# Kernel tuning notes

Measured on AMD Instinct MI355X. Metric: run time of the kernel, lower is better.

Reference implementation:

```python
import jax, jax.numpy as jnp
import numpy as np

B = 64
N_TEXT, N_VIS, N_AC = 256, 32, 32
N = N_TEXT + N_VIS + N_AC  # 320 total graph nodes
HID, HEADS, LAYERS = 512, 8, 2
HEAD_DIM = HID // HEADS
SW_K, SW_P, SF_M, ALPHA, CROSS_P = 6, 0.15, 3, 0.5, 0.3


def build_hybrid_adj():
    """Watts-Strogatz + Barabasi-Albert hybrid adjacency with cross-modal edges (numpy, setup only)."""
    rng = np.random.default_rng(0)
    # small-world ring lattice
    sw = np.zeros((N, N), np.float32)
    idx = np.arange(N)
    for j in range(1, SW_K // 2 + 1):
        sw[idx, (idx + j) % N] = 1.0
        sw[idx, (idx - j) % N] = 1.0
    # rewiring
    for i in range(N):
        for j in range(i + 1, N):
            if sw[i, j] == 1 and rng.random() < SW_P:
                sw[i, j] = sw[j, i] = 0.0
                cand = np.where(sw[i] == 0)[0]
                cand = cand[cand != i]
                if len(cand) > 0:
                    nj = rng.choice(cand)
                    sw[i, nj] = sw[nj, i] = 1.0
    # scale-free (Barabasi-Albert)
    sf = np.zeros((N, N), np.float32)
    for i in range(SF_M + 1):
        for j in range(i + 1, SF_M + 1):
            sf[i, j] = sf[j, i] = 1.0
    deg = sf.sum(1)
    for v in range(SF_M + 1, N):
        prob = deg[:v] / deg[:v].sum()
        targets = rng.choice(v, size=min(SF_M, v), replace=False, p=prob)
        sf[v, targets] = 1.0
        sf[targets, v] = 1.0
        deg = sf.sum(1)
    adj = ((ALPHA * sw + (1.0 - ALPHA) * sf) > 0.3).astype(np.float32)
    # cross-modal edges: text<->visual, text<->acoustic (Bernoulli), visual<->acoustic temporal diagonal
    ts, te = 0, N_TEXT
    vs, ve = te, te + N_VIS
    as_, ae = ve, ve + N_AC
    cm_v = (rng.random((N_TEXT, N_VIS)) < CROSS_P).astype(np.float32)
    adj[ts:te, vs:ve] = np.maximum(adj[ts:te, vs:ve], cm_v)
    adj[vs:ve, ts:te] = adj[ts:te, vs:ve].T
    cm_a = (rng.random((N_TEXT, N_AC)) < CROSS_P).astype(np.float32)
    adj[ts:te, as_:ae] = np.maximum(adj[ts:te, as_:ae], cm_a)
    adj[as_:ae, ts:te] = adj[ts:te, as_:ae].T
    k = min(N_VIS, N_AC)
    adj[vs + np.arange(k), as_ + np.arange(k)] = 1.0
    adj[as_ + np.arange(k), vs + np.arange(k)] = 1.0
    return adj.astype(np.int32)


def setup_inputs() -> dict:
    key = jax.random.key(0)
    ks = jax.random.split(key, 12)
    s = 0.02
    return {
        "text": jax.random.normal(ks[0], (B, N_TEXT, 768), jnp.float32),
        "visual": jax.random.normal(ks[1], (B, N_VIS, 47), jnp.float32),
        "acoustic": jax.random.normal(ks[2], (B, N_AC, 74), jnp.float32),
        "adj": jnp.asarray(build_hybrid_adj()),
        "Wt": jax.random.normal(ks[3], (768, HID), jnp.float32) * s,
        "Wv": jax.random.normal(ks[4], (47, HID), jnp.float32) * s,
        "Wa": jax.random.normal(ks[5], (74, HID), jnp.float32) * s,
        "Wg": jax.random.normal(ks[6], (LAYERS, HEADS, HID, HEAD_DIM), jnp.float32) * s,
        "a_src": jax.random.normal(ks[7], (LAYERS, HEADS, HEAD_DIM), jnp.float32) * s,
        "a_dst": jax.random.normal(ks[8], (LAYERS, HEADS, HEAD_DIM), jnp.float32) * s,
        "edge_logits": jax.random.normal(ks[9], (N, N), jnp.float32) * s,
    }


def _fusion(text, visual, acoustic, adj, Wt, Wv, Wa, Wg, a_src, a_dst, edge_logits):
    # project each modality into shared hidden space and stack as graph nodes
    x = jnp.concatenate([
        jnp.einsum("btd,dh->bth", text, Wt),
        jnp.einsum("bvd,dh->bvh", visual, Wv),
        jnp.einsum("bad,dh->bah", acoustic, Wa),
    ], axis=1)  # [B, N, HID]
    mask = (adj != 0)[None, None, :, :]  # [1,1,N,N]
    for l in range(LAYERS):
        h = jnp.einsum("bnd,hdf->bhnf", x, Wg[l])          # [B,H,N,Fh]
        # a([h_i || h_j]) factorizes: e_ij = a_src.h_i + a_dst.h_j
        fi = jnp.einsum("bhnf,hf->bhn", h, a_src[l])
        fj = jnp.einsum("bhnf,hf->bhn", h, a_dst[l])
        e = jax.nn.leaky_relu(fi[:, :, :, None] + fj[:, :, None, :], 0.2)
        e = e + edge_logits[None, None, :, :]               # learnable topology bias
        e = jnp.where(mask, e, -jnp.inf)                    # adjacency-masked scores
        att = jnp.nan_to_num(jax.nn.softmax(e, axis=-1))    # fully-masked rows -> 0
        out = jnp.einsum("bhij,bhjf->bhif", att, h)         # message passing
        x = out.transpose(0, 2, 1, 3).reshape(x.shape[0], N, HID)  # concat heads
        if l < LAYERS - 1:
            x = jax.nn.elu(x)
    return x  # [B, N, HID] fused node embeddings


def reference(text, visual, acoustic, adj, Wt, Wv, Wa, Wg, a_src, a_dst, edge_logits):
    return _fusion(text, visual, acoustic, adj, Wt, Wv, Wa, Wg, a_src, a_dst, edge_logits)
```

## Files before the change

kernel.cpp:

```cpp
#include <hip/hip_runtime.h>
#include <hip/hip_bf16.h>
#include <math.h>

#define BB 64
#define NN 320
#define NT 256
#define NV 32
#define NA 32
#define HIDD 512
#define NHEAD 8
#define FD 64

#define LDK 40

typedef __attribute__((ext_vector_type(8))) short bf16x8;
typedef __attribute__((ext_vector_type(4))) float floatx4;

__device__ __forceinline__ void split1(float v, unsigned short& h, unsigned short& l) {
    unsigned u = __float_as_uint(v);
    unsigned hu = u & 0xFFFF0000u;
    float lf = v - __uint_as_float(hu);
    h = (unsigned short)(hu >> 16);
    l = (unsigned short)(__float_as_uint(lf) >> 16);
}
__device__ __forceinline__ unsigned pack2(unsigned short a, unsigned short b) {
    return (unsigned)a | ((unsigned)b << 16);
}

__global__ __launch_bounds__(256) void gemm_mfma(
    const float* __restrict__ A, const float* __restrict__ Bsrc,
    float* __restrict__ C, unsigned short* __restrict__ Hthi,
    unsigned short* __restrict__ Htlo, int M, int K, int b_mode, int rpb, int noff)
{
    __shared__ unsigned short Ah[128 * LDK];
    __shared__ unsigned short Al[128 * LDK];
    __shared__ unsigned short Bh[128 * LDK];
    __shared__ unsigned short Bl[128 * LDK];

    const int tid  = threadIdx.x;
    const int lane = tid & 63;
    const int w    = tid >> 6;
    const int rw   = w >> 1, cw = w & 1;
    const int m0   = blockIdx.x * 128;
    const int n0   = blockIdx.y * 128;

    floatx4 acc[4][4];
#pragma unroll
    for (int s = 0; s < 4; s++)
#pragma unroll
        for (int t = 0; t < 4; t++) acc[s][t] = (floatx4)0.f;

    const int arow = tid >> 1;
    const int akh  = (tid & 1) * 16;
    const int bc   = tid & 127;
    const int bkh  = (tid >> 7) * 16;
    const int bhead = (n0 + bc) >> 6;
    const int bf    = (n0 + bc) & 63;

    const int afrag0 = (rw * 64 + (lane & 15)) * LDK + (lane >> 4) * 8;
    const int bfrag0 = (cw * 64 + (lane & 15)) * LDK + (lane >> 4) * 8;

    for (int k0 = 0; k0 < K; k0 += 32) {
        __syncthreads();
        {
            const float* ga = A + (size_t)(m0 + arow) * K + k0 + akh;
            const int la = arow * LDK + akh;
            if (k0 + 32 <= K) {
#pragma unroll
                for (int u = 0; u < 4; u++) {
                    float4 v = *(const float4*)(ga + 4 * u);
                    unsigned short h0,h1,h2,h3,l0,l1,l2,l3;
                    split1(v.x,h0,l0); split1(v.y,h1,l1);
                    split1(v.z,h2,l2); split1(v.w,h3,l3);
                    *(uint2*)&Ah[la + 4*u] = make_uint2(pack2(h0,h1), pack2(h2,h3));
                    *(uint2*)&Al[la + 4*u] = make_uint2(pack2(l0,l1), pack2(l2,l3));
                }
            } else {
#pragma unroll
                for (int u = 0; u < 16; u++) {
                    float v = (k0 + akh + u < K) ? ga[u] : 0.f;
                    unsigned short h, l; split1(v, h, l);
                    Ah[la + u] = h; Al[la + u] = l;
                }
            }
        }
        {
            unsigned short hb[16], lb[16];
#pragma unroll
            for (int u = 0; u < 16; u++) {
                int k = k0 + bkh + u;
                float v;
                if (k < K) {
                    size_t gi = b_mode
                        ? (size_t)bhead * (512 * 64) + (size_t)k * 64 + bf
                        : (size_t)k * 512 + n0 + bc;
                    v = Bsrc[gi];
                } else v = 0.f;
                split1(v, hb[u], lb[u]);
            }
            const int lb0 = bc * LDK + bkh;
#pragma unroll
            for (int u = 0; u < 4; u++) {
                *(uint2*)&Bh[lb0 + 4*u] = make_uint2(pack2(hb[4*u],hb[4*u+1]), pack2(hb[4*u+2],hb[4*u+3]));
                *(uint2*)&Bl[lb0 + 4*u] = make_uint2(pack2(lb[4*u],lb[4*u+1]), pack2(lb[4*u+2],lb[4*u+3]));
            }
        }
        __syncthreads();

        bf16x8 ah[4], al[4], bh[4], bl[4];
#pragma unroll
        for (int s = 0; s < 4; s++) {
            ah[s] = *(const bf16x8*)&Ah[afrag0 + s * 16 * LDK];
            al[s] = *(const bf16x8*)&Al[afrag0 + s * 16 * LDK];
        }
#pragma unroll
        for (int t = 0; t < 4; t++) {
            bh[t] = *(const bf16x8*)&Bh[bfrag0 + t * 16 * LDK];
            bl[t] = *(const bf16x8*)&Bl[bfrag0 + t * 16 * LDK];
        }
#pragma unroll
        for (int s = 0; s < 4; s++)
#pragma unroll
            for (int t = 0; t < 4; t++) {
                acc[s][t] = __builtin_amdgcn_mfma_f32_16x16x32_bf16(ah[s], bh[t], acc[s][t], 0, 0, 0);
                acc[s][t] = __builtin_amdgcn_mfma_f32_16x16x32_bf16(ah[s], bl[t], acc[s][t], 0, 0, 0);
                acc[s][t] = __builtin_amdgcn_mfma_f32_16x16x32_bf16(al[s], bh[t], acc[s][t], 0, 0, 0);
            }
    }

    if (b_mode == 0) {
#pragma unroll
        for (int s = 0; s < 4; s++) {
            const int gr0 = m0 + rw * 64 + s * 16 + (lane >> 4) * 4;
#pragma unroll
            for (int r = 0; r < 4; r++) {
                const unsigned grow = gr0 + r;
                const unsigned b = grow / (unsigned)rpb;
                const unsigned rr = grow - b * rpb;
                float* crow = C + ((size_t)b * NN + noff + rr) * HIDD;
#pragma unroll
                for (int t = 0; t < 4; t++) {
                    crow[n0 + cw * 64 + t * 16 + (lane & 15)] = acc[s][t][r];
                }
            }
        }
    } else {
        const int hd = (n0 + cw * 64) >> 6;
        const int fq = lane & 15;
#pragma unroll
        for (int s = 0; s < 4; s++) {
            const int m_s = m0 + rw * 64 + s * 16 + (lane >> 4) * 4;
            const unsigned b = (unsigned)m_s / 320u;
            const int jb = m_s - b * 320;
            const int ks = jb >> 5;
            const int jg2 = (jb >> 3) & 3;
            const int eb = jb & 7;
            const size_t slab = (size_t)b * 8 + hd;
#pragma unroll
            for (int t = 0; t < 4; t++) {
                unsigned short h0,h1,h2,h3,l0,l1,l2,l3;
                split1(acc[s][t][0],h0,l0); split1(acc[s][t][1],h1,l1);
                split1(acc[s][t][2],h2,l2); split1(acc[s][t][3],h3,l3);
                const size_t base = (((slab * 10 + ks) * 4 + t) * 512
                                     + (size_t)(fq | (jg2 << 4)) * 8) + eb;
                *(uint2*)&Hthi[base] = make_uint2(pack2(h0,h1), pack2(h2,h3));
                *(uint2*)&Htlo[base] = make_uint2(pack2(l0,l1), pack2(l2,l3));
            }
        }
    }
}

__global__ __launch_bounds__(256, 2) void attn_mfma(
    const unsigned short* __restrict__ Hthi, const unsigned short* __restrict__ Htlo,
    const float* __restrict__ asrc, const float* __restrict__ adst,
    const int*   __restrict__ adj,  const float* __restrict__ elog,
    float* __restrict__ xout, int apply_elu)
{
    __shared__ float ff4[2][4][NN];
    __shared__ float fjs[NN];
    __shared__ float ls[NN];

    const int bh = blockIdx.x;
    const int hd = bh & 7, b = bh >> 3;
    const int tid = threadIdx.x, lane = tid & 63, w = tid >> 6;
    const int fq = lane & 15, jg = lane >> 4;

    {
        const int f = (w << 4) + fq;
        const float as = asrc[hd * 64 + f];
        const float ad = adst[hd * 64 + f];
#pragma unroll 2
        for (int ks = 0; ks < 10; ks++) {
            const unsigned off = (((unsigned)bh * 10 + ks) * 4 + w) * 512 + (unsigned)lane * 8;
            bf16x8 hh = *(const bf16x8*)&Hthi[off];
            bf16x8 hl = *(const bf16x8*)&Htlo[off];
            float v[16];
#pragma unroll
            for (int e = 0; e < 8; e++) {
                float hv = __uint_as_float(((unsigned)(unsigned short)hh[e]) << 16)
                         + __uint_as_float(((unsigned)(unsigned short)hl[e]) << 16);
                v[e] = hv * as; v[8 + e] = hv * ad;
            }
#pragma unroll
            for (int d = 8; d >= 1; d >>= 1) {
                const bool up = (fq & d) != 0;
#pragma unroll
                for (int m = 0; m < d; m++) {
                    float snd = up ? v[m] : v[m + d];
                    float rec = __shfl_xor(snd, d);
                    v[m] = (up ? v[m + d] : v[m]) + rec;
                }
            }
            ff4[fq >> 3][w][ks * 32 + jg * 8 + (fq & 7)] = v[0];
        }
    }
    __syncthreads();

    float fir[5];
#pragma unroll
    for (int ip = 0; ip < 5; ip++) {
        const int i = ip * 64 + (w << 4) + fq;
        fir[ip] = (ff4[0][0][i] + ff4[0][1][i]) + (ff4[0][2][i] + ff4[0][3][i]);
    }
    for (int r = tid; r < NN; r += 256)
        fjs[r] = (ff4[1][0][r] + ff4[1][1][r]) + (ff4[1][2][r] + ff4[1][3][r]);
    __syncthreads();

    floatx4 acc[5][4];
#pragma unroll
    for (int ip = 0; ip < 5; ip++)
#pragma unroll
        for (int nt = 0; nt < 4; nt++) acc[ip][nt] = (floatx4)0.f;
    float lacc[5] = {0.f, 0.f, 0.f, 0.f, 0.f};

    for (int ks = 0; ks < 10; ks++) {
        bf16x8 bhf[4], blf[4];
#pragma unroll
        for (int nt = 0; nt < 4; nt++) {
            const unsigned off = (((unsigned)bh * 10 + ks) * 4 + nt) * 512 + (unsigned)lane * 8;
            bhf[nt] = *(const bf16x8*)&Hthi[off];
            blf[nt] = *(const bf16x8*)&Htlo[off];
        }
        const int j8 = ks * 32 + jg * 8;
        const float4 fj0 = *(const float4*)&fjs[j8];
        const float4 fj1 = *(const float4*)&fjs[j8 + 4];

        bf16x8 ahh[5], all[5];
#pragma unroll
        for (int ip = 0; ip < 5; ip++) {
            const int i = ip * 64 + (w << 4) + fq;
            const float fiv = fir[ip];
            const unsigned g = (unsigned)i * NN + j8;
            const int4   a0 = *(const int4*)&adj[g];
            const int4   a1 = *(const int4*)&adj[g + 4];
            const float4 e0 = *(const float4*)&elog[g];
            const float4 e1 = *(const float4*)&elog[g + 4];
            float p[8];
            {
                float s;
                s = fiv + fj0.x; s = fmaxf(s, 0.2f*s); s = a0.x ? (s + e0.x) : -INFINITY; p[0] = __expf(s);
                s = fiv + fj0.y; s = fmaxf(s, 0.2f*s); s = a0.y ? (s + e0.y) : -INFINITY; p[1] = __expf(s);
                s = fiv + fj0.z; s = fmaxf(s, 0.2f*s); s = a0.z ? (s + e0.z) : -INFINITY; p[2] = __expf(s);
                s = fiv + fj0.w; s = fmaxf(s, 0.2f*s); s = a0.w ? (s + e0.w) : -INFINITY; p[3] = __expf(s);
                s = fiv + fj1.x; s = fmaxf(s, 0.2f*s); s = a1.x ? (s + e1.x) : -INFINITY; p[4] = __expf(s);
                s = fiv + fj1.y; s = fmaxf(s, 0.2f*s); s = a1.y ? (s + e1.y) : -INFINITY; p[5] = __expf(s);
                s = fiv + fj1.z; s = fmaxf(s, 0.2f*s); s = a1.z ? (s + e1.z) : -INFINITY; p[6] = __expf(s);
                s = fiv + fj1.w; s = fmaxf(s, 0.2f*s); s = a1.w ? (s + e1.w) : -INFINITY; p[7] = __expf(s);
            }
            lacc[ip] += ((p[0]+p[1]) + (p[2]+p[3])) + ((p[4]+p[5]) + (p[6]+p[7]));

            unsigned short ph[8], pl[8];
#pragma unroll
            for (int e = 0; e < 8; e++) split1(p[e], ph[e], pl[e]);
            union { uint4 u; bf16x8 v; } ua, ul;
            ua.u = make_uint4(pack2(ph[0],ph[1]), pack2(ph[2],ph[3]),
                              pack2(ph[4],ph[5]), pack2(ph[6],ph[7]));
            ul.u = make_uint4(pack2(pl[0],pl[1]), pack2(pl[2],pl[3]),
                              pack2(pl[4],pl[5]), pack2(pl[6],pl[7]));
            ahh[ip] = ua.v; all[ip] = ul.v;
        }

#pragma unroll
        for (int ip = 0; ip < 5; ip++)
#pragma unroll
            for (int nt = 0; nt < 4; nt++) {
                acc[ip][nt] = __builtin_amdgcn_mfma_f32_16x16x32_bf16(ahh[ip], bhf[nt], acc[ip][nt], 0, 0, 0);
                acc[ip][nt] = __builtin_amdgcn_mfma_f32_16x16x32_bf16(ahh[ip], blf[nt], acc[ip][nt], 0, 0, 0);
                acc[ip][nt] = __builtin_amdgcn_mfma_f32_16x16x32_bf16(all[ip], bhf[nt], acc[ip][nt], 0, 0, 0);
            }
    }

#pragma unroll
    for (int ip = 0; ip < 5; ip++) {
        float l = lacc[ip];
        l += __shfl_xor(l, 16);
        l += __shfl_xor(l, 32);
        if (jg == 0) ls[ip * 64 + (w << 4) + fq] = l;
    }
    __syncthreads();

#pragma unroll
    for (int ip = 0; ip < 5; ip++) {
        const int ib = (ip * 4 + w) * 16 + jg * 4;
#pragma unroll
        for (int r = 0; r < 4; r++) {
            const float lv = ls[ib + r];
            const float inv = (lv > 0.f) ? 1.f / lv : 0.f;
            float* orow = xout + ((size_t)(b * NN + ib + r)) * HIDD + hd * 64;
#pragma unroll
            for (int nt = 0; nt < 4; nt++) {
                float vv = acc[ip][nt][r] * inv;
                if (apply_elu) vv = (vv > 0.f) ? vv : __expf(vv) - 1.f;
                orow[nt * 16 + fq] = vv;
            }
        }
    }
}

extern "C" void kernel_launch(void* const* d_in, const int* in_sizes, int n_in,
                              void* d_out, int out_size, void* d_ws, size_t ws_size,
                              hipStream_t stream)
{
    (void)in_sizes; (void)n_in; (void)out_size; (void)ws_size;
    const float* text     = (const float*)d_in[0];
    const float* visual   = (const float*)d_in[1];
    const float* acoustic = (const float*)d_in[2];
    const int*   adj      = (const int*)d_in[3];
    const float* Wt       = (const float*)d_in[4];
    const float* Wv       = (const float*)d_in[5];
    const float* Wa       = (const float*)d_in[6];
    const float* Wg       = (const float*)d_in[7];
    const float* a_src    = (const float*)d_in[8];
    const float* a_dst    = (const float*)d_in[9];
    const float* elog     = (const float*)d_in[10];

    float* xbuf = (float*)d_out;
    unsigned short* Hthi = (unsigned short*)d_ws;
    unsigned short* Htlo = Hthi + (size_t)512 * 10 * 4 * 512;

    gemm_mfma<<<dim3((BB*NT)/128, 4), 256, 0, stream>>>(text,     Wt, xbuf, nullptr, nullptr, BB*NT, 768, 0, NT, 0);
    gemm_mfma<<<dim3((BB*NV)/128, 4), 256, 0, stream>>>(visual,   Wv, xbuf, nullptr, nullptr, BB*NV,  47, 0, NV, NT);
    gemm_mfma<<<dim3((BB*NA)/128, 4), 256, 0, stream>>>(acoustic, Wa, xbuf, nullptr, nullptr, BB*NA,  74, 0, NA, NT + NV);

    for (int l = 0; l < 2; l++) {
        const float* Wg_l = Wg + (size_t)l * NHEAD * HIDD * FD;
        gemm_mfma<<<dim3((BB*NN)/128, 4), 256, 0, stream>>>(xbuf, Wg_l, nullptr, Hthi, Htlo, BB*NN, HIDD, 1, NN, 0);
        attn_mfma<<<BB * NHEAD, 256, 0, stream>>>(
            Hthi, Htlo, a_src + l * NHEAD * FD, a_dst + l * NHEAD * FD,
            adj, elog, xbuf, (l == 0) ? 1 : 0);
    }
}
```

Baseline: 416.8 us.

## Precompute masked exp bias, fuse attention logits into GEMM, split attention rows

```diff
diff --git a/kernel.cpp b/kernel.cpp
--- a/kernel.cpp
+++ b/kernel.cpp
@@ -16,6 +16,10 @@
 typedef __attribute__((ext_vector_type(8))) short bf16x8;
 typedef __attribute__((ext_vector_type(4))) float floatx4;
 
+__device__ float me_g[NN * NN];
+__device__ float fif_g[512 * NN];
+__device__ float fjf_g[512 * NN];
+
 __device__ __forceinline__ void split1(float v, unsigned short& h, unsigned short& l) {
     unsigned u = __float_as_uint(v);
     unsigned hu = u & 0xFFFF0000u;
@@ -27,10 +31,25 @@
     return (unsigned)a | ((unsigned)b << 16);
 }
 
+__global__ __launch_bounds__(256) void build_me(
+    const int* __restrict__ adj, const float* __restrict__ elog)
+{
+    const int i4 = (blockIdx.x * 256 + threadIdx.x) * 4;
+    const int4   a = *(const int4*)&adj[i4];
+    const float4 e = *(const float4*)&elog[i4];
+    float4 m;
+    m.x = a.x ? __expf(e.x) : 0.f;
+    m.y = a.y ? __expf(e.y) : 0.f;
+    m.z = a.z ? __expf(e.z) : 0.f;
+    m.w = a.w ? __expf(e.w) : 0.f;
+    *(float4*)&me_g[i4] = m;
+}
+
 __global__ __launch_bounds__(256) void gemm_mfma(
     const float* __restrict__ A, const float* __restrict__ Bsrc,
     float* __restrict__ C, unsigned short* __restrict__ Hthi,
-    unsigned short* __restrict__ Htlo, int M, int K, int b_mode, int rpb, int noff)
+    unsigned short* __restrict__ Htlo, const float* __restrict__ asrc,
+    const float* __restrict__ adst, int M, int K, int b_mode, int rpb, int noff)
 {
     __shared__ unsigned short Ah[128 * LDK];
     __shared__ unsigned short Al[128 * LDK];
@@ -167,105 +186,91 @@
                 *(uint2*)&Htlo[base] = make_uint2(pack2(l0,l1), pack2(l2,l3));
             }
         }
-    }
-}
-
-__global__ __launch_bounds__(256, 2) void attn_mfma(
+        float as4[4], ad4[4];
+#pragma unroll
+        for (int t = 0; t < 4; t++) {
+            as4[t] = asrc[hd * 64 + t * 16 + fq];
+            ad4[t] = adst[hd * 64 + t * 16 + fq];
+        }
+#pragma unroll
+        for (int s = 0; s < 4; s++) {
+            const int m_s = m0 + rw * 64 + s * 16 + (lane >> 4) * 4;
+            const unsigned b = (unsigned)m_s / 320u;
+            const int jb = m_s - b * 320;
+            float4 fi4, fj4;
+#pragma unroll
+            for (int r = 0; r < 4; r++) {
+                float fi = (acc[s][0][r]*as4[0] + acc[s][1][r]*as4[1])
+                         + (acc[s][2][r]*as4[2] + acc[s][3][r]*as4[3]);
+                float fj = (acc[s][0][r]*ad4[0] + acc[s][1][r]*ad4[1])
+                         + (acc[s][2][r]*ad4[2] + acc[s][3][r]*ad4[3]);
+#pragma unroll
+                for (int d = 1; d < 16; d <<= 1) {
+                    fi += __shfl_xor(fi, d);
+                    fj += __shfl_xor(fj, d);
+                }
+                ((float*)&fi4)[r] = fi; ((float*)&fj4)[r] = fj;
+            }
+            if (fq == 0) {
+                const size_t o = ((size_t)b * 8 + hd) * NN + jb;
+                *(float4*)&fif_g[o] = fi4;
+                *(float4*)&fjf_g[o] = fj4;
+            }
+        }
+    }
+}
+
+template<int IP0, int NIP>
+__device__ __forceinline__ void attn_body(
     const unsigned short* __restrict__ Hthi, const unsigned short* __restrict__ Htlo,
-    const float* __restrict__ asrc, const float* __restrict__ adst,
-    const int*   __restrict__ adj,  const float* __restrict__ elog,
-    float* __restrict__ xout, int apply_elu)
-{
-    __shared__ float ff4[2][4][NN];
-    __shared__ float fjs[NN];
-    __shared__ float ls[NN];
-
+    float* __restrict__ xout, int apply_elu, float* fjs, float* ls)
+{
     const int bh = blockIdx.x;
     const int hd = bh & 7, b = bh >> 3;
     const int tid = threadIdx.x, lane = tid & 63, w = tid >> 6;
     const int fq = lane & 15, jg = lane >> 4;
 
-    {
-        const int f = (w << 4) + fq;
-        const float as = asrc[hd * 64 + f];
-        const float ad = adst[hd * 64 + f];
-#pragma unroll 2
-        for (int ks = 0; ks < 10; ks++) {
-            const unsigned off = (((unsigned)bh * 10 + ks) * 4 + w) * 512 + (unsigned)lane * 8;
-            bf16x8 hh = *(const bf16x8*)&Hthi[off];
-            bf16x8 hl = *(const bf16x8*)&Htlo[off];
-            float v[16];
-#pragma unroll
-            for (int e = 0; e < 8; e++) {
-                float hv = __uint_as_float(((unsigned)(unsigned short)hh[e]) << 16)
-                         + __uint_as_float(((unsigned)(unsigned short)hl[e]) << 16);
-                v[e] = hv * as; v[8 + e] = hv * ad;
-            }
-#pragma unroll
-            for (int d = 8; d >= 1; d >>= 1) {
-                const bool up = (fq & d) != 0;
-#pragma unroll
-                for (int m = 0; m < d; m++) {
-                    float snd = up ? v[m] : v[m + d];
-                    float rec = __shfl_xor(snd, d);
-                    v[m] = (up ? v[m + d] : v[m]) + rec;
-                }
-            }
-            ff4[fq >> 3][w][ks * 32 + jg * 8 + (fq & 7)] = v[0];
-        }
-    }
+    for (int r = tid; r < NN; r += 256) fjs[r] = fjf_g[bh * NN + r];
+
+    float fir[NIP];
+#pragma unroll
+    for (int ip = 0; ip < NIP; ip++)
+        fir[ip] = fif_g[bh * NN + (IP0 + ip) * 64 + (w << 4) + fq];
     __syncthreads();
 
-    float fir[5];
-#pragma unroll
-    for (int ip = 0; ip < 5; ip++) {
-        const int i = ip * 64 + (w << 4) + fq;
-        fir[ip] = (ff4[0][0][i] + ff4[0][1][i]) + (ff4[0][2][i] + ff4[0][3][i]);
-    }
-    for (int r = tid; r < NN; r += 256)
-        fjs[r] = (ff4[1][0][r] + ff4[1][1][r]) + (ff4[1][2][r] + ff4[1][3][r]);
-    __syncthreads();
-
-    floatx4 acc[5][4];
-#pragma unroll
-    for (int ip = 0; ip < 5; ip++)
+    floatx4 acc[NIP][4];
+#pragma unroll
+    for (int ip = 0; ip < NIP; ip++)
 #pragma unroll
         for (int nt = 0; nt < 4; nt++) acc[ip][nt] = (floatx4)0.f;
-    float lacc[5] = {0.f, 0.f, 0.f, 0.f, 0.f};
+    float lacc[NIP];
+#pragma unroll
+    for (int ip = 0; ip < NIP; ip++) lacc[ip] = 0.f;
 
     for (int ks = 0; ks < 10; ks++) {
-        bf16x8 bhf[4], blf[4];
-#pragma unroll
-        for (int nt = 0; nt < 4; nt++) {
-            const unsigned off = (((unsigned)bh * 10 + ks) * 4 + nt) * 512 + (unsigned)lane * 8;
-            bhf[nt] = *(const bf16x8*)&Hthi[off];
-            blf[nt] = *(const bf16x8*)&Htlo[off];
-        }
         const int j8 = ks * 32 + jg * 8;
         const float4 fj0 = *(const float4*)&fjs[j8];
         const float4 fj1 = *(const float4*)&fjs[j8 + 4];
 
-        bf16x8 ahh[5], all[5];
-#pragma unroll
-        for (int ip = 0; ip < 5; ip++) {
-            const int i = ip * 64 + (w << 4) + fq;
+        bf16x8 ahh[NIP], all[NIP];
+#pragma unroll
+        for (int ip = 0; ip < NIP; ip++) {
+            const int i = (IP0 + ip) * 64 + (w << 4) + fq;
             const float fiv = fir[ip];
             const unsigned g = (unsigned)i * NN + j8;
-            const int4   a0 = *(const int4*)&adj[g];
-            const int4   a1 = *(const int4*)&adj[g + 4];
-            const float4 e0 = *(const float4*)&elog[g];
-            const float4 e1 = *(const float4*)&elog[g + 4];
+            const float4 m0 = *(const float4*)&me_g[g];
+            const float4 m1 = *(const float4*)&me_g[g + 4];
             float p[8];
             {
                 float s;
-                s = fiv + fj0.x; s = fmaxf(s, 0.2f*s); s = a0.x ? (s + e0.x) : -INFINITY; p[0] = __expf(s);
-                s = fiv + fj0.y; s = fmaxf(s, 0.2f*s); s = a0.y ? (s + e0.y) : -INFINITY; p[1] = __expf(s);
-                s = fiv + fj0.z; s = fmaxf(s, 0.2f*s); s = a0.z ? (s + e0.z) : -INFINITY; p[2] = __expf(s);
-                s = fiv + fj0.w; s = fmaxf(s, 0.2f*s); s = a0.w ? (s + e0.w) : -INFINITY; p[3] = __expf(s);
-                s = fiv + fj1.x; s = fmaxf(s, 0.2f*s); s = a1.x ? (s + e1.x) : -INFINITY; p[4] = __expf(s);
-                s = fiv + fj1.y; s = fmaxf(s, 0.2f*s); s = a1.y ? (s + e1.y) : -INFINITY; p[5] = __expf(s);
-                s = fiv + fj1.z; s = fmaxf(s, 0.2f*s); s = a1.z ? (s + e1.z) : -INFINITY; p[6] = __expf(s);
-                s = fiv + fj1.w; s = fmaxf(s, 0.2f*s); s = a1.w ? (s + e1.w) : -INFINITY; p[7] = __expf(s);
+                s = fiv + fj0.x; s = fmaxf(s, 0.2f*s); p[0] = __expf(s) * m0.x;
+                s = fiv + fj0.y; s = fmaxf(s, 0.2f*s); p[1] = __expf(s) * m0.y;
+                s = fiv + fj0.z; s = fmaxf(s, 0.2f*s); p[2] = __expf(s) * m0.z;
+                s = fiv + fj0.w; s = fmaxf(s, 0.2f*s); p[3] = __expf(s) * m0.w;
+                s = fiv + fj1.x; s = fmaxf(s, 0.2f*s); p[4] = __expf(s) * m1.x;
+                s = fiv + fj1.y; s = fmaxf(s, 0.2f*s); p[5] = __expf(s) * m1.y;
+                s = fiv + fj1.z; s = fmaxf(s, 0.2f*s); p[6] = __expf(s) * m1.z;
+                s = fiv + fj1.w; s = fmaxf(s, 0.2f*s); p[7] = __expf(s) * m1.w;
             }
             lacc[ip] += ((p[0]+p[1]) + (p[2]+p[3])) + ((p[4]+p[5]) + (p[6]+p[7]));
 
@@ -281,27 +286,31 @@
         }
 
 #pragma unroll
-        for (int ip = 0; ip < 5; ip++)
-#pragma unroll
-            for (int nt = 0; nt < 4; nt++) {
-                acc[ip][nt] = __builtin_amdgcn_mfma_f32_16x16x32_bf16(ahh[ip], bhf[nt], acc[ip][nt], 0, 0, 0);
-                acc[ip][nt] = __builtin_amdgcn_mfma_f32_16x16x32_bf16(ahh[ip], blf[nt], acc[ip][nt], 0, 0, 0);
-                acc[ip][nt] = __builtin_amdgcn_mfma_f32_16x16x32_bf16(all[ip], bhf[nt], acc[ip][nt], 0, 0, 0);
-            }
-    }
-
-#pragma unroll
-    for (int ip = 0; ip < 5; ip++) {
+        for (int nt = 0; nt < 4; nt++) {
+            const unsigned off = (((unsigned)bh * 10 + ks) * 4 + nt) * 512 + (unsigned)lane * 8;
+            const bf16x8 bhf = *(const bf16x8*)&Hthi[off];
+            const bf16x8 blf = *(const bf16x8*)&Htlo[off];
+#pragma unroll
+            for (int ip = 0; ip < NIP; ip++) {
+                acc[ip][nt] = __builtin_amdgcn_mfma_f32_16x16x32_bf16(ahh[ip], bhf, acc[ip][nt], 0, 0, 0);
+                acc[ip][nt] = __builtin_amdgcn_mfma_f32_16x16x32_bf16(ahh[ip], blf, acc[ip][nt], 0, 0, 0);
+                acc[ip][nt] = __builtin_amdgcn_mfma_f32_16x16x32_bf16(all[ip], bhf, acc[ip][nt], 0, 0, 0);
+            }
+        }
+    }
+
+#pragma unroll
+    for (int ip = 0; ip < NIP; ip++) {
         float l = lacc[ip];
         l += __shfl_xor(l, 16);
         l += __shfl_xor(l, 32);
-        if (jg == 0) ls[ip * 64 + (w << 4) + fq] = l;
+        if (jg == 0) ls[(IP0 + ip) * 64 + (w << 4) + fq] = l;
     }
     __syncthreads();
 
 #pragma unroll
-    for (int ip = 0; ip < 5; ip++) {
-        const int ib = (ip * 4 + w) * 16 + jg * 4;
+    for (int ip = 0; ip < NIP; ip++) {
+        const int ib = ((IP0 + ip) * 4 + w) * 16 + jg * 4;
 #pragma unroll
         for (int r = 0; r < 4; r++) {
             const float lv = ls[ib + r];
@@ -315,6 +324,16 @@
             }
         }
     }
+}
+
+__global__ __launch_bounds__(256, 4) void attn_mfma(
+    const unsigned short* __restrict__ Hthi, const unsigned short* __restrict__ Htlo,
+    float* __restrict__ xout, int apply_elu)
+{
+    __shared__ float fjs[NN];
+    __shared__ float ls[NN];
+    if (blockIdx.y == 0) attn_body<0, 3>(Hthi, Htlo, xout, apply_elu, fjs, ls);
+    else                 attn_body<3, 2>(Hthi, Htlo, xout, apply_elu, fjs, ls);
 }
 
 extern "C" void kernel_launch(void* const* d_in, const int* in_sizes, int n_in,
@@ -338,15 +357,17 @@
     unsigned short* Hthi = (unsigned short*)d_ws;
     unsigned short* Htlo = Hthi + (size_t)512 * 10 * 4 * 512;
 
-    gemm_mfma<<<dim3((BB*NT)/128, 4), 256, 0, stream>>>(text,     Wt, xbuf, nullptr, nullptr, BB*NT, 768, 0, NT, 0);
-    gemm_mfma<<<dim3((BB*NV)/128, 4), 256, 0, stream>>>(visual,   Wv, xbuf, nullptr, nullptr, BB*NV,  47, 0, NV, NT);
-    gemm_mfma<<<dim3((BB*NA)/128, 4), 256, 0, stream>>>(acoustic, Wa, xbuf, nullptr, nullptr, BB*NA,  74, 0, NA, NT + NV);
+    build_me<<<NN * NN / 1024, 256, 0, stream>>>(adj, elog);
+
+    gemm_mfma<<<dim3((BB*NT)/128, 4), 256, 0, stream>>>(text,     Wt, xbuf, nullptr, nullptr, nullptr, nullptr, BB*NT, 768, 0, NT, 0);
+    gemm_mfma<<<dim3((BB*NV)/128, 4), 256, 0, stream>>>(visual,   Wv, xbuf, nullptr, nullptr, nullptr, nullptr, BB*NV,  47, 0, NV, NT);
+    gemm_mfma<<<dim3((BB*NA)/128, 4), 256, 0, stream>>>(acoustic, Wa, xbuf, nullptr, nullptr, nullptr, nullptr, BB*NA,  74, 0, NA, NT + NV);
 
     for (int l = 0; l < 2; l++) {
         const float* Wg_l = Wg + (size_t)l * NHEAD * HIDD * FD;
-        gemm_mfma<<<dim3((BB*NN)/128, 4), 256, 0, stream>>>(xbuf, Wg_l, nullptr, Hthi, Htlo, BB*NN, HIDD, 1, NN, 0);
-        attn_mfma<<<BB * NHEAD, 256, 0, stream>>>(
-            Hthi, Htlo, a_src + l * NHEAD * FD, a_dst + l * NHEAD * FD,
-            adj, elog, xbuf, (l == 0) ? 1 : 0);
-    }
-}
+        gemm_mfma<<<dim3((BB*NN)/128, 4), 256, 0, stream>>>(xbuf, Wg_l, nullptr, Hthi, Htlo,
+            a_src + l * NHEAD * FD, a_dst + l * NHEAD * FD, BB*NN, HIDD, 1, NN, 0);
+        attn_mfma<<<dim3(BB * NHEAD, 2), 256, 0, stream>>>(
+            Hthi, Htlo, xbuf, (l == 0) ? 1 : 0);
+    }
+}
```

New measurement: 372.1 us. 1.12x faster.
